# Performance work log

Measured on AMD Instinct MI355X. Metric: run time of the kernel, lower is better.

## Reference

```python
import jax, jax.numpy as jnp
import numpy as np

EPS = 1e-5

def _layer_norm(x, w, b):
    mu = jnp.mean(x, axis=-1, keepdims=True)
    var = jnp.mean(jnp.square(x - mu), axis=-1, keepdims=True)
    return (x - mu) * jax.lax.rsqrt(var + EPS) * w + b

def setup_inputs() -> dict:
    key = jax.random.key(0)
    ks = jax.random.split(key, 5)
    B, S, C = 1, 512, 128
    scale = 1.0 / np.sqrt(C)
    return {
        "z_ij": jax.random.normal(ks[0], (B, S, S, C), dtype=jnp.float32),
        "ln_w": jnp.ones((C,), jnp.float32),
        "ln_b": jnp.zeros((C,), jnp.float32),
        "wa": jax.random.normal(ks[1], (C, C), dtype=jnp.float32) * scale,
        "wb": jax.random.normal(ks[2], (C, C), dtype=jnp.float32) * scale,
        "wg": jax.random.normal(ks[3], (C, C), dtype=jnp.float32) * scale,
        "fln_w": jnp.ones((C,), jnp.float32),
        "fln_b": jnp.zeros((C,), jnp.float32),
        "wf": jax.random.normal(ks[4], (C, C), dtype=jnp.float32) * scale,
    }

def reference(z_ij, ln_w, ln_b, wa, wb, wg, fln_w, fln_b, wf):
    # z_ij: (B, S, S, C). torch Linear(x) == x @ W.T
    z = _layer_norm(z_ij, ln_w, ln_b)
    a = jax.nn.sigmoid(z @ wa.T)  # (B, S, S, C)
    b = jax.nn.sigmoid(z @ wb.T)
    g = jax.nn.sigmoid(z @ wg.T)
    # torch: einsum('...kic,...kjc->...ijc', a.transpose(-3,-2), b)
    # == out[i,j,c] = sum_k a[i,k,c] * b[k,j,c]
    p = jnp.einsum('bikc,bkjc->bijc', a, b)
    return g * (_layer_norm(p, fln_w, fln_b) @ wf.T)
```

## Files before the change

kernel.cpp:

```cpp
#include <hip/hip_runtime.h>

#define SS 512
#define CC 128
#define RR (SS*SS)

typedef unsigned short u16;
typedef unsigned int   u32;
typedef __attribute__((ext_vector_type(4))) float f32x4;
typedef __attribute__((ext_vector_type(8))) short s16x8;
typedef __attribute__((ext_vector_type(4))) u32   u32x4;

__device__ __forceinline__ float bf2f(u16 u){ u32 x = ((u32)u)<<16; float f; __builtin_memcpy(&f,&x,4); return f; }
__device__ __forceinline__ float sigf(float x){ return 1.f/(1.f + __expf(-x)); }

__device__ __forceinline__ u32 cvtpk(float lo, float hi){
  u32 r; asm("v_cvt_pk_bf16_f32 %0, %1, %2" : "=v"(r) : "v"(lo), "v"(hi)); return r;
}

typedef __attribute__((address_space(1))) void* gptr_t;
typedef __attribute__((address_space(3))) void* lptr_t;
__device__ __forceinline__ void load_lds16(const void* g, void* l){
  __builtin_amdgcn_global_load_lds((gptr_t)(g), (lptr_t)(l), 16, 0, 0);
}

__global__ void k0(const float* __restrict__ wa, const float* __restrict__ wb,
                   const float* __restrict__ wg, const float* __restrict__ wf,
                   u16* __restrict__ wabg, u16* __restrict__ wfbg)
{
  int t = blockIdx.x*256 + threadIdx.x;
  const float* srcs[4] = {wa, wb, wg, wf};
  int m = t >> 11;
  int e = (t & 2047) * 8;
  const float* s = srcs[m] + e;
  u32 pk[4];
  #pragma unroll
  for (int v=0; v<2; v++){
    f32x4 x = *reinterpret_cast<const f32x4*>(s + v*4);
    pk[v*2]   = cvtpk(x[0], x[1]);
    pk[v*2+1] = cvtpk(x[2], x[3]);
  }
  u16* dst = (m==3) ? (wfbg + e) : (wabg + m*16384 + e);
  *reinterpret_cast<u32x4*>(dst) = *reinterpret_cast<u32x4*>(pk);
}

__global__ __launch_bounds__(256,4) void k1(
    const float* __restrict__ z, const float* __restrict__ lnw, const float* __restrict__ lnb,
    const u16* __restrict__ wabg,
    u16* __restrict__ a_t, u16* __restrict__ b_t, u16* __restrict__ g_out,
    float* __restrict__ SaPart)
{
  __shared__ __align__(16) u16 un[9216];
  __shared__ __align__(16) u16 wk[64*128];
  u16 (*zn)[136] = reinterpret_cast<u16(*)[136]>(un);
  u16* tr = un;
  const int tid = threadIdx.x;
  const int r0  = blockIdx.x * 64;
  const int lane = tid & 63, w = tid >> 6;
  const int iI   = r0 >> 9;
  const int kblk = (r0 >> 6) & 7;

  auto stageW = [&](int m, int h){
    const u16* Wb = wabg + m*16384 + h*8192;
    #pragma unroll
    for (int s=0;s<4;s++){
      int lr = s*16 + (tid>>4);
      const u16* gsrc = Wb + lr*128 + (((tid&15) ^ (lr&7))<<3);
      load_lds16((const void*)gsrc, (void*)&wk[s*2048 + w*512]);
    }
  };

  stageW(0,0);

  {
    int row = tid >> 2, q = tid & 3;
    const float* src = z + (size_t)(r0+row)*CC + q*32;
    float v[32]; float s = 0.f, s2 = 0.f;
    #pragma unroll
    for (int i=0;i<8;i++){
      f32x4 t = *reinterpret_cast<const f32x4*>(src + i*4);
      #pragma unroll
      for (int e=0;e<4;e++){ float x = t[e]; v[i*4+e]=x; s += x; s2 += x*x; }
    }
    s  += __shfl_xor(s,1);  s2 += __shfl_xor(s2,1);
    s  += __shfl_xor(s,2);  s2 += __shfl_xor(s2,2);
    float mu  = s * (1.f/128.f);
    float var = s2*(1.f/128.f) - mu*mu;
    float rs  = rsqrtf(var + 1e-5f);
    #pragma unroll
    for (int i=0;i<4;i++){
      u32 pk[4];
      #pragma unroll
      for (int e=0;e<8;e+=2){
        int ci = i*8+e; int c = q*32 + ci;
        float y0 = (v[ci]  -mu)*rs*lnw[c]   + lnb[c];
        float y1 = (v[ci+1]-mu)*rs*lnw[c+1] + lnb[c+1];
        pk[e>>1] = cvtpk(y0, y1);
      }
      *reinterpret_cast<u32x4*>(&zn[row][q*32 + i*8]) = *reinterpret_cast<u32x4*>(pk);
    }
  }
  __syncthreads();

  s16x8 af[4];
  #pragma unroll
  for (int ks=0;ks<4;ks++)
    af[ks] = *reinterpret_cast<const s16x8*>(&zn[w*16 + (lane&15)][ks*32 + (lane>>4)*8]);

  for (int m=0;m<3;m++){
    f32x4 acc[8];
    #pragma unroll
    for (int cb=0;cb<8;cb++) acc[cb] = (f32x4){0.f,0.f,0.f,0.f};

    #pragma unroll
    for (int cb=0;cb<4;cb++){
      int lr = cb*16 + (lane&15);
      const int rx = (lr&7)<<3;
      const u16* base = &wk[lr*128];
      s16x8 b0 = *reinterpret_cast<const s16x8*>(&base[(  0 + (lane>>4)*8) ^ rx]);
      s16x8 b1 = *reinterpret_cast<const s16x8*>(&base[( 32 + (lane>>4)*8) ^ rx]);
      s16x8 b2 = *reinterpret_cast<const s16x8*>(&base[( 64 + (lane>>4)*8) ^ rx]);
      s16x8 b3 = *reinterpret_cast<const s16x8*>(&base[( 96 + (lane>>4)*8) ^ rx]);
      acc[cb] = __builtin_amdgcn_mfma_f32_16x16x32_bf16(af[0], b0, acc[cb], 0,0,0);
      acc[cb] = __builtin_amdgcn_mfma_f32_16x16x32_bf16(af[1], b1, acc[cb], 0,0,0);
      acc[cb] = __builtin_amdgcn_mfma_f32_16x16x32_bf16(af[2], b2, acc[cb], 0,0,0);
      acc[cb] = __builtin_amdgcn_mfma_f32_16x16x32_bf16(af[3], b3, acc[cb], 0,0,0);
    }
    __syncthreads();
    stageW(m,1);
    __syncthreads();

    #pragma unroll
    for (int cb=4;cb<8;cb++){
      int lr = (cb-4)*16 + (lane&15);
      const int rx = (lr&7)<<3;
      const u16* base = &wk[lr*128];
      s16x8 b0 = *reinterpret_cast<const s16x8*>(&base[(  0 + (lane>>4)*8) ^ rx]);
      s16x8 b1 = *reinterpret_cast<const s16x8*>(&base[( 32 + (lane>>4)*8) ^ rx]);
      s16x8 b2 = *reinterpret_cast<const s16x8*>(&base[( 64 + (lane>>4)*8) ^ rx]);
      s16x8 b3 = *reinterpret_cast<const s16x8*>(&base[( 96 + (lane>>4)*8) ^ rx]);
      acc[cb] = __builtin_amdgcn_mfma_f32_16x16x32_bf16(af[0], b0, acc[cb], 0,0,0);
      acc[cb] = __builtin_amdgcn_mfma_f32_16x16x32_bf16(af[1], b1, acc[cb], 0,0,0);
      acc[cb] = __builtin_amdgcn_mfma_f32_16x16x32_bf16(af[2], b2, acc[cb], 0,0,0);
      acc[cb] = __builtin_amdgcn_mfma_f32_16x16x32_bf16(af[3], b3, acc[cb], 0,0,0);
    }
    __syncthreads();

    if (m<2) stageW(m+1,0);

    if (m < 2){
      #pragma unroll
      for (int cb=0;cb<8;cb++){
        int col = cb*16 + (lane&15);
        int rbase = w*16 + (lane>>4)*4;
        u32 p0 = cvtpk(sigf(acc[cb][0])-0.5f, sigf(acc[cb][1])-0.5f);
        u32 p1 = cvtpk(sigf(acc[cb][2])-0.5f, sigf(acc[cb][3])-0.5f);
        u32* d = reinterpret_cast<u32*>(&tr[col*72 + rbase]);
        d[0] = p0; d[1] = p1;
      }
      asm volatile("s_waitcnt lgkmcnt(0)" ::: "memory");
      __builtin_amdgcn_s_barrier();
      {
        int c = tid>>1, half = tid&1;
        u16* dst = (m==0 ? a_t : b_t) + ((size_t)c<<18) + r0 + half*32;
        const u16* srcl = &tr[c*72 + half*32];
        float s = 0.f;
        #pragma unroll
        for (int e=0;e<4;e++){
          u32x4 t = *reinterpret_cast<const u32x4*>(srcl + e*8);
          *reinterpret_cast<u32x4*>(dst + e*8) = t;
          #pragma unroll
          for (int q=0;q<4;q++){ u32 v = t[q]; s += bf2f((u16)v) + bf2f((u16)(v>>16)); }
        }
        if (m==0){
          s += __shfl_xor(s, 1);
          if ((tid&1)==0) SaPart[(kblk<<16) + (iI<<7) + c] = s;
        }
      }
      __syncthreads();
    } else {
      u16* gb = &tr[0];
      #pragma unroll
      for (int cb=0;cb<8;cb++){
        int col = cb*16 + (lane&15);
        int rbase = w*16 + (lane>>4)*4;
        #pragma unroll
        for (int q=0;q<4;q++){
          float sg = sigf(acc[cb][q]);
          gb[(rbase+q)*136 + col] = (u16)cvtpk(sg, sg);
        }
      }
      asm volatile("s_waitcnt lgkmcnt(0)" ::: "memory");
      __builtin_amdgcn_s_barrier();
      {
        int row = tid>>2, qo = tid&3;
        u16* dst = g_out + (size_t)(r0+row)*CC + qo*32;
        const u16* srcl = &gb[row*136 + qo*32];
        #pragma unroll
        for (int e=0;e<4;e++)
          *reinterpret_cast<u32x4*>(dst + e*8) = *reinterpret_cast<const u32x4*>(srcl + e*8);
      }
    }
  }
}

__global__ __launch_bounds__(256,4) void k1b(const u16* __restrict__ b_t, u16* __restrict__ bT,
                                             float* __restrict__ SbPart)
{
  __shared__ __align__(16) u16 tile[64][72];
  const int tid = threadIdx.x;
  const int c  = blockIdx.x >> 6;
  const int t  = blockIdx.x & 63;
  const int k0 = (t>>3)*64, j0 = (t&7)*64;
  const u16* src = b_t + ((size_t)c<<18);
  {
    int row = tid>>3, chunk = tid&7;
    #pragma unroll
    for (int pass=0; pass<2; pass++){
      int k = row + pass*32;
      const u16* s = src + (size_t)(k0+k)*SS + j0 + chunk*8;
      u32x4 v = *reinterpret_cast<const u32x4*>(s);
      int cs = chunk ^ ((k>>3)&7);
      *reinterpret_cast<u32x4*>(&tile[k][cs*8]) = v;
    }
  }
  __syncthreads();
  {
    int j = tid>>2, part = tid&3;
    u32 pk[8];
    float sb = 0.f;
    #pragma unroll
    for (int i=0;i<16;i+=2){
      int ka = part*16 + i;
      int key = (ka>>3)&7;
      u16 va = tile[ka  ][(((j>>3)^key)*8) + (j&7)];
      u16 vb = tile[ka+1][(((j>>3)^key)*8) + (j&7)];
      pk[i>>1] = (u32)va | ((u32)vb<<16);
      sb += bf2f(va) + bf2f(vb);
    }
    u16* dst = bT + ((size_t)c<<18) + (size_t)(j0+j)*SS + k0 + part*16;
    *reinterpret_cast<u32x4*>(dst)   = *reinterpret_cast<u32x4*>(pk);
    *reinterpret_cast<u32x4*>(dst+8) = *reinterpret_cast<u32x4*>(pk+4);
    sb += __shfl_xor(sb, 1);
    sb += __shfl_xor(sb, 2);
    if (part==0) SbPart[(((c<<9) + j0 + j)<<3) + (k0>>6)] = sb;
  }
}

__global__ void k1c(const float* __restrict__ SaPart, const float* __restrict__ SbPart,
                    float* __restrict__ Sa, float* __restrict__ Sb)
{
  int idx = blockIdx.x*256 + threadIdx.x;
  if (idx < 65536){
    int i = idx >> 7, c = idx & 127;
    float s = 0.f;
    #pragma unroll
    for (int b=0;b<8;b++) s += SaPart[(b<<16) + (i<<7) + c];
    Sa[(c<<9) + i] = s;
  } else {
    int cj = idx & 65535;
    const float* src = SbPart + ((size_t)cj << 3);
    float s = 0.f;
    #pragma unroll
    for (int b=0;b<8;b++) s += src[b];
    Sb[cj] = s;
  }
}

__global__ __launch_bounds__(256,2) void k2(const u16* __restrict__ a_t, const u16* __restrict__ bT,
                                            const float* __restrict__ Sa, const float* __restrict__ Sb,
                                            _Float16* __restrict__ ph)
{
  __shared__ __align__(16) u16 As[2][128*64];
  __shared__ __align__(16) u16 Bs[128*64];
  const int tid = threadIdx.x;
  const int lane = tid & 63, w = tid >> 6;
  const int bid = blockIdx.x;
  const int swz = (bid & 7) * 256 + (bid >> 3);
  const int c   = swz >> 4;
  const int t16 = swz & 15;
  const int i0 = (t16 >> 2) * 128, j0 = (t16 & 3) * 128;
  const u16* Ag = a_t + ((size_t)c<<18);
  const u16* Bg = bT  + ((size_t)c<<18);
  const int pr = lane>>3, slot = lane&7;

  auto stageA = [&](int kt, int buf){
    #pragma unroll
    for (int s=0;s<4;s++){
      int rbase = w*32 + s*8;
      int rl = rbase + pr;
      const u16* g = Ag + (size_t)(i0+rl)*SS + kt*64 + ((slot^pr)*8);
      load_lds16((const void*)g, (void*)&As[buf][rbase*64]);
    }
  };
  auto stageB = [&](int kt){
    #pragma unroll
    for (int s=0;s<4;s++){
      int rbase = w*32 + s*8;
      int rl = rbase + pr;
      const u16* g = Bg + (size_t)(j0+rl)*SS + kt*64 + ((slot^pr)*8);
      load_lds16((const void*)g, (void*)&Bs[rbase*64]);
    }
  };

  f32x4 acc[4][4];
  #pragma unroll
  for (int a=0;a<4;a++)
    #pragma unroll
    for (int b=0;b<4;b++) acc[a][b] = (f32x4){0.f,0.f,0.f,0.f};
  const int wr = w>>1, wc = w&1;

  stageA(0, 0);
  for (int kt=0; kt<8; ++kt){
    stageB(kt);
    if (kt < 7){
      stageA(kt+1, (kt+1)&1);
      asm volatile("s_waitcnt vmcnt(4)" ::: "memory");
    } else {
      asm volatile("s_waitcnt vmcnt(0)" ::: "memory");
    }
    __builtin_amdgcn_s_barrier();
    const u16* Ab = &As[kt&1][0];
    #pragma unroll
    for (int ks=0;ks<2;ks++){
      s16x8 af[4], bfv[4];
      #pragma unroll
      for (int f=0; f<4; f++){
        int i = wr*64 + f*16 + (lane&15);
        int ch = (ks*4 + (lane>>4)) ^ (i&7);
        af[f] = *reinterpret_cast<const s16x8*>(&Ab[i*64 + ch*8]);
        int j = wc*64 + f*16 + (lane&15);
        int chb = (ks*4 + (lane>>4)) ^ (j&7);
        bfv[f] = *reinterpret_cast<const s16x8*>(&Bs[j*64 + chb*8]);
      }
      #pragma unroll
      for (int fi=0;fi<4;fi++)
        #pragma unroll
        for (int fj=0;fj<4;fj++)
          acc[fi][fj] = __builtin_amdgcn_mfma_f32_16x16x32_bf16(af[fi], bfv[fj], acc[fi][fj], 0,0,0);
    }
    asm volatile("s_waitcnt lgkmcnt(0)" ::: "memory");
    __builtin_amdgcn_s_barrier();
  }

  _Float16* P = ph + ((size_t)c<<18);
  const float* SaC = Sa + (c<<9);
  const float* SbC = Sb + (c<<9);
  float sbv[4];
  #pragma unroll
  for (int fj=0;fj<4;fj++) sbv[fj] = SbC[j0 + wc*64 + fj*16 + (lane&15)];
  #pragma unroll
  for (int fi=0;fi<4;fi++){
    int rbase = i0 + wr*64 + fi*16 + (lane>>4)*4;
    #pragma unroll
    for (int q=0;q<4;q++){
      float sav = SaC[rbase+q];
      #pragma unroll
      for (int fj=0;fj<4;fj++){
        int col = j0 + wc*64 + fj*16 + (lane&15);
        P[(size_t)(rbase+q)*SS + col] = (_Float16)(0.5f*(sav + sbv[fj]) + acc[fi][fj][q]);
      }
    }
  }
}

__global__ __launch_bounds__(256,3) void k3(const _Float16* __restrict__ ph, const u16* __restrict__ g,
    const float* __restrict__ flnw, const float* __restrict__ flnb,
    const u16* __restrict__ wfbg, float* __restrict__ out)
{
  __shared__ __align__(16) u16 znp[64][136];
  __shared__ __align__(16) u16 wk[128*128];
  __shared__ __align__(16) float red[4][64];
  __shared__ __align__(16) float muv[64], rsv[64];
  const int tid = threadIdx.x;
  const int rr0 = blockIdx.x * 64;
  const int lane = tid&63, w = tid>>6;
  const int pos = tid & 63, cq = tid >> 6;

  {
    #pragma unroll
    for (int s=0;s<8;s++){
      int row = s*16 + (tid>>4);
      const u16* gsrc = wfbg + row*128 + (((tid&15) ^ (row&7))<<3);
      load_lds16((const void*)gsrc, (void*)&wk[s*2048 + w*512]);
    }
  }

  float pv[32];
  {
    const _Float16* src = ph + rr0 + pos;
    float s = 0.f;
    #pragma unroll
    for (int ci=0;ci<32;ci++){
      int c = cq*32 + ci;
      float x = (float)src[((size_t)c)<<18];
      pv[ci] = x; s += x;
    }
    red[cq][pos] = s;
  }
  __syncthreads();
  if (tid < 64) muv[tid] = (red[0][tid]+red[1][tid]+red[2][tid]+red[3][tid]) * (1.f/128.f);
  __syncthreads();
  float mu = muv[pos];
  {
    float s2 = 0.f;
    #pragma unroll
    for (int ci=0;ci<32;ci++){ float d = pv[ci]-mu; s2 += d*d; }
    red[cq][pos] = s2;
  }
  __syncthreads();
  if (tid < 64) rsv[tid] = rsqrtf((red[0][tid]+red[1][tid]+red[2][tid]+red[3][tid])*(1.f/128.f) + 1e-5f);
  __syncthreads();
  float rs = rsv[pos];
  {
    u32 pk[4];
    #pragma unroll
    for (int ii=0;ii<4;ii++){
      #pragma unroll
      for (int e=0;e<8;e+=2){
        int ci = ii*8+e; int c = cq*32+ci;
        float y0 = (pv[ci]  -mu)*rs*flnw[c]   + flnb[c];
        float y1 = (pv[ci+1]-mu)*rs*flnw[c+1] + flnb[c+1];
        pk[e>>1] = cvtpk(y0, y1);
      }
      *reinterpret_cast<u32x4*>(&znp[pos][cq*32 + ii*8]) = *reinterpret_cast<u32x4*>(pk);
    }
  }
  __syncthreads();

  f32x4 acc[8];
  #pragma unroll
  for (int cb=0;cb<8;cb++) acc[cb] = (f32x4){0.f,0.f,0.f,0.f};
  #pragma unroll
  for (int ks=0;ks<4;ks++){
    s16x8 af = *reinterpret_cast<const s16x8*>(&znp[w*16 + (lane&15)][ks*32 + (lane>>4)*8]);
    #pragma unroll
    for (int cb=0;cb<8;cb++){
      int row = cb*16 + (lane&15);
      const int rx = (row&7)<<3;
      s16x8 bf = *reinterpret_cast<const s16x8*>(&wk[row*128 + ((ks*32 + (lane>>4)*8) ^ rx)]);
      acc[cb] = __builtin_amdgcn_mfma_f32_16x16x32_bf16(af, bf, acc[cb], 0,0,0);
    }
  }
  __syncthreads();

  u16* gb = &znp[0][0];
  {
    int row = tid>>2, qo = tid&3;
    const u16* src = g + (size_t)(rr0+row)*CC + qo*32;
    #pragma unroll
    for (int e=0;e<4;e++)
      *reinterpret_cast<u32x4*>(&gb[row*136 + qo*32 + e*8]) = *reinterpret_cast<const u32x4*>(src + e*8);
  }
  __syncthreads();
  #pragma unroll
  for (int cb=0;cb<8;cb++){
    int col = cb*16 + (lane&15);
    int rbase = w*16 + (lane>>4)*4;
    #pragma unroll
    for (int q=0;q<4;q++){
      float gv = bf2f(gb[(rbase+q)*136 + col]);
      out[(size_t)(rr0+rbase+q)*CC + col] = gv * acc[cb][q];
    }
  }
}

extern "C" void kernel_launch(void* const* d_in, const int* in_sizes, int n_in,
                              void* d_out, int out_size, void* d_ws, size_t ws_size,
                              hipStream_t stream)
{
  const float* z    = (const float*)d_in[0];
  const float* lnw  = (const float*)d_in[1];
  const float* lnb  = (const float*)d_in[2];
  const float* wa   = (const float*)d_in[3];
  const float* wb   = (const float*)d_in[4];
  const float* wg   = (const float*)d_in[5];
  const float* flnw = (const float*)d_in[6];
  const float* flnb = (const float*)d_in[7];
  const float* wf   = (const float*)d_in[8];
  float* out = (float*)d_out;

  char* ws = (char*)d_ws;
  u16* a_t = (u16*)(ws);
  u16* bT  = (u16*)(ws + ((size_t)64<<20));
  u16* g   = (u16*)(ws + ((size_t)128<<20));
  _Float16* ph = (_Float16*)(ws + ((size_t)192<<20));
  u16* b_t = (u16*)(ws + ((size_t)192<<20));
  u16* wfbg = (u16*)(ws + ((size_t)256<<20));

  char* ob = (char*)d_out;
  u16*   wabg   = (u16*)ob;
  float* SaPart = (float*)(ob + ((size_t)1<<20));
  float* SbPart = (float*)(ob + ((size_t)3<<20));
  float* Sa     = (float*)(ob + ((size_t)5<<20));
  float* Sb     = (float*)(ob + ((size_t)5<<20) + ((size_t)256<<10));

  k0 <<<32,   256, 0, stream>>>(wa, wb, wg, wf, wabg, wfbg);
  k1 <<<4096, 256, 0, stream>>>(z, lnw, lnb, wabg, a_t, b_t, g, SaPart);
  k1b<<<8192, 256, 0, stream>>>(b_t, bT, SbPart);
  k1c<<<512,  256, 0, stream>>>(SaPart, SbPart, Sa, Sb);
  k2 <<<2048, 256, 0, stream>>>(a_t, bT, Sa, Sb, ph);
  k3 <<<4096, 256, 0, stream>>>(ph, g, flnw, flnb, wfbg, out);
}
```

Measured before the change: 276.6 us.

## Shrink weight LDS staging in k1/k3 and raise occupancy launch bounds

k1 now streams each 128x128 gate weight into LDS in four 32-row quarters instead of two 64-row halves, and k3 streams Wf in two halves instead of all at once. Both changes shrink the shared-memory footprint so more blocks can be resident per CU. Launch-bound minimum-occupancy hints are raised on k1, k1b, k2 and k3. The cost is more barriers and weight reloads that are exposed without overlap, plus a risk of register spills under the tighter register limits.

Result: slower. 296.4 us (+7.1%).

```diff
diff --git a/kernel.cpp b/kernel.cpp
--- a/kernel.cpp
+++ b/kernel.cpp
@@ -43,14 +43,14 @@
   *reinterpret_cast<u32x4*>(dst) = *reinterpret_cast<u32x4*>(pk);
 }
 
-__global__ __launch_bounds__(256,4) void k1(
+__global__ __launch_bounds__(256,6) void k1(
     const float* __restrict__ z, const float* __restrict__ lnw, const float* __restrict__ lnb,
     const u16* __restrict__ wabg,
     u16* __restrict__ a_t, u16* __restrict__ b_t, u16* __restrict__ g_out,
     float* __restrict__ SaPart)
 {
   __shared__ __align__(16) u16 un[9216];
-  __shared__ __align__(16) u16 wk[64*128];
+  __shared__ __align__(16) u16 wk[32*128];
   u16 (*zn)[136] = reinterpret_cast<u16(*)[136]>(un);
   u16* tr = un;
   const int tid = threadIdx.x;
@@ -59,10 +59,10 @@
   const int iI   = r0 >> 9;
   const int kblk = (r0 >> 6) & 7;
 
-  auto stageW = [&](int m, int h){
-    const u16* Wb = wabg + m*16384 + h*8192;
-    #pragma unroll
-    for (int s=0;s<4;s++){
+  auto stageW = [&](int m, int qt){
+    const u16* Wb = wabg + m*16384 + qt*4096;
+    #pragma unroll
+    for (int s=0;s<2;s++){
       int lr = s*16 + (tid>>4);
       const u16* gsrc = Wb + lr*128 + (((tid&15) ^ (lr&7))<<3);
       load_lds16((const void*)gsrc, (void*)&wk[s*2048 + w*512]);
@@ -111,41 +111,26 @@
     #pragma unroll
     for (int cb=0;cb<8;cb++) acc[cb] = (f32x4){0.f,0.f,0.f,0.f};
 
-    #pragma unroll
-    for (int cb=0;cb<4;cb++){
-      int lr = cb*16 + (lane&15);
-      const int rx = (lr&7)<<3;
-      const u16* base = &wk[lr*128];
-      s16x8 b0 = *reinterpret_cast<const s16x8*>(&base[(  0 + (lane>>4)*8) ^ rx]);
-      s16x8 b1 = *reinterpret_cast<const s16x8*>(&base[( 32 + (lane>>4)*8) ^ rx]);
-      s16x8 b2 = *reinterpret_cast<const s16x8*>(&base[( 64 + (lane>>4)*8) ^ rx]);
-      s16x8 b3 = *reinterpret_cast<const s16x8*>(&base[( 96 + (lane>>4)*8) ^ rx]);
-      acc[cb] = __builtin_amdgcn_mfma_f32_16x16x32_bf16(af[0], b0, acc[cb], 0,0,0);
-      acc[cb] = __builtin_amdgcn_mfma_f32_16x16x32_bf16(af[1], b1, acc[cb], 0,0,0);
-      acc[cb] = __builtin_amdgcn_mfma_f32_16x16x32_bf16(af[2], b2, acc[cb], 0,0,0);
-      acc[cb] = __builtin_amdgcn_mfma_f32_16x16x32_bf16(af[3], b3, acc[cb], 0,0,0);
-    }
-    __syncthreads();
-    stageW(m,1);
-    __syncthreads();
-
-    #pragma unroll
-    for (int cb=4;cb<8;cb++){
-      int lr = (cb-4)*16 + (lane&15);
-      const int rx = (lr&7)<<3;
-      const u16* base = &wk[lr*128];
-      s16x8 b0 = *reinterpret_cast<const s16x8*>(&base[(  0 + (lane>>4)*8) ^ rx]);
-      s16x8 b1 = *reinterpret_cast<const s16x8*>(&base[( 32 + (lane>>4)*8) ^ rx]);
-      s16x8 b2 = *reinterpret_cast<const s16x8*>(&base[( 64 + (lane>>4)*8) ^ rx]);
-      s16x8 b3 = *reinterpret_cast<const s16x8*>(&base[( 96 + (lane>>4)*8) ^ rx]);
-      acc[cb] = __builtin_amdgcn_mfma_f32_16x16x32_bf16(af[0], b0, acc[cb], 0,0,0);
-      acc[cb] = __builtin_amdgcn_mfma_f32_16x16x32_bf16(af[1], b1, acc[cb], 0,0,0);
-      acc[cb] = __builtin_amdgcn_mfma_f32_16x16x32_bf16(af[2], b2, acc[cb], 0,0,0);
-      acc[cb] = __builtin_amdgcn_mfma_f32_16x16x32_bf16(af[3], b3, acc[cb], 0,0,0);
-    }
-    __syncthreads();
-
-    if (m<2) stageW(m+1,0);
+    for (int qt=0; qt<4; ++qt){
+      __syncthreads();
+      #pragma unroll
+      for (int cc=0; cc<2; ++cc){
+        int cb = qt*2 + cc;
+        int lr = cc*16 + (lane&15);
+        const int rx = (lr&7)<<3;
+        const u16* base = &wk[lr*128];
+        s16x8 b0 = *reinterpret_cast<const s16x8*>(&base[(  0 + (lane>>4)*8) ^ rx]);
+        s16x8 b1 = *reinterpret_cast<const s16x8*>(&base[( 32 + (lane>>4)*8) ^ rx]);
+        s16x8 b2 = *reinterpret_cast<const s16x8*>(&base[( 64 + (lane>>4)*8) ^ rx]);
+        s16x8 b3 = *reinterpret_cast<const s16x8*>(&base[( 96 + (lane>>4)*8) ^ rx]);
+        acc[cb] = __builtin_amdgcn_mfma_f32_16x16x32_bf16(af[0], b0, acc[cb], 0,0,0);
+        acc[cb] = __builtin_amdgcn_mfma_f32_16x16x32_bf16(af[1], b1, acc[cb], 0,0,0);
+        acc[cb] = __builtin_amdgcn_mfma_f32_16x16x32_bf16(af[2], b2, acc[cb], 0,0,0);
+        acc[cb] = __builtin_amdgcn_mfma_f32_16x16x32_bf16(af[3], b3, acc[cb], 0,0,0);
+      }
+      __syncthreads();
+      if (qt<3) stageW(m, qt+1);
+    }
 
     if (m < 2){
       #pragma unroll
@@ -157,8 +142,8 @@
         u32* d = reinterpret_cast<u32*>(&tr[col*72 + rbase]);
         d[0] = p0; d[1] = p1;
       }
-      asm volatile("s_waitcnt lgkmcnt(0)" ::: "memory");
-      __builtin_amdgcn_s_barrier();
+      __syncthreads();
+      stageW(m+1, 0);
       {
         int c = tid>>1, half = tid&1;
         u16* dst = (m==0 ? a_t : b_t) + ((size_t)c<<18) + r0 + half*32;
@@ -189,8 +174,7 @@
           gb[(rbase+q)*136 + col] = (u16)cvtpk(sg, sg);
         }
       }
-      asm volatile("s_waitcnt lgkmcnt(0)" ::: "memory");
-      __builtin_amdgcn_s_barrier();
+      __syncthreads();
       {
         int row = tid>>2, qo = tid&3;
         u16* dst = g_out + (size_t)(r0+row)*CC + qo*32;
@@ -203,7 +187,7 @@
   }
 }
 
-__global__ __launch_bounds__(256,4) void k1b(const u16* __restrict__ b_t, u16* __restrict__ bT,
+__global__ __launch_bounds__(256,8) void k1b(const u16* __restrict__ b_t, u16* __restrict__ bT,
                                              float* __restrict__ SbPart)
 {
   __shared__ __align__(16) u16 tile[64][72];
@@ -266,7 +250,7 @@
   }
 }
 
-__global__ __launch_bounds__(256,2) void k2(const u16* __restrict__ a_t, const u16* __restrict__ bT,
+__global__ __launch_bounds__(256,3) void k2(const u16* __restrict__ a_t, const u16* __restrict__ bT,
                                             const float* __restrict__ Sa, const float* __restrict__ Sb,
                                             _Float16* __restrict__ ph)
 {
@@ -363,12 +347,12 @@
   }
 }
 
-__global__ __launch_bounds__(256,3) void k3(const _Float16* __restrict__ ph, const u16* __restrict__ g,
+__global__ __launch_bounds__(256,4) void k3(const _Float16* __restrict__ ph, const u16* __restrict__ g,
     const float* __restrict__ flnw, const float* __restrict__ flnb,
     const u16* __restrict__ wfbg, float* __restrict__ out)
 {
   __shared__ __align__(16) u16 znp[64][136];
-  __shared__ __align__(16) u16 wk[128*128];
+  __shared__ __align__(16) u16 wk[64*128];
   __shared__ __align__(16) float red[4][64];
   __shared__ __align__(16) float muv[64], rsv[64];
   const int tid = threadIdx.x;
@@ -376,14 +360,17 @@
   const int lane = tid&63, w = tid>>6;
   const int pos = tid & 63, cq = tid >> 6;
 
-  {
-    #pragma unroll
-    for (int s=0;s<8;s++){
-      int row = s*16 + (tid>>4);
-      const u16* gsrc = wfbg + row*128 + (((tid&15) ^ (row&7))<<3);
+  auto stageWF = [&](int h){
+    const u16* Wb = wfbg + h*8192;
+    #pragma unroll
+    for (int s=0;s<4;s++){
+      int lr = s*16 + (tid>>4);
+      const u16* gsrc = Wb + lr*128 + (((tid&15) ^ (lr&7))<<3);
       load_lds16((const void*)gsrc, (void*)&wk[s*2048 + w*512]);
     }
-  }
+  };
+
+  stageWF(0);
 
   float pv[32];
   {
@@ -430,14 +417,30 @@
   f32x4 acc[8];
   #pragma unroll
   for (int cb=0;cb<8;cb++) acc[cb] = (f32x4){0.f,0.f,0.f,0.f};
+
   #pragma unroll
   for (int ks=0;ks<4;ks++){
     s16x8 af = *reinterpret_cast<const s16x8*>(&znp[w*16 + (lane&15)][ks*32 + (lane>>4)*8]);
     #pragma unroll
-    for (int cb=0;cb<8;cb++){
-      int row = cb*16 + (lane&15);
-      const int rx = (row&7)<<3;
-      s16x8 bf = *reinterpret_cast<const s16x8*>(&wk[row*128 + ((ks*32 + (lane>>4)*8) ^ rx)]);
+    for (int cb=0;cb<4;cb++){
+      int lr = cb*16 + (lane&15);
+      const int rx = (lr&7)<<3;
+      s16x8 bf = *reinterpret_cast<const s16x8*>(&wk[lr*128 + ((ks*32 + (lane>>4)*8) ^ rx)]);
+      acc[cb] = __builtin_amdgcn_mfma_f32_16x16x32_bf16(af, bf, acc[cb], 0,0,0);
+    }
+  }
+  __syncthreads();
+  stageWF(1);
+  __syncthreads();
+
+  #pragma unroll
+  for (int ks=0;ks<4;ks++){
+    s16x8 af = *reinterpret_cast<const s16x8*>(&znp[w*16 + (lane&15)][ks*32 + (lane>>4)*8]);
+    #pragma unroll
+    for (int cb=4;cb<8;cb++){
+      int lr = (cb-4)*16 + (lane&15);
+      const int rx = (lr&7)<<3;
+      s16x8 bf = *reinterpret_cast<const s16x8*>(&wk[lr*128 + ((ks*32 + (lane>>4)*8) ^ rx)]);
       acc[cb] = __builtin_amdgcn_mfma_f32_16x16x32_bf16(af, bf, acc[cb], 0,0,0);
     }
   }
```

## Store gate in channel-major layout and raise occupancy bounds on k1b and k2

Applied to the files above, without the earlier changes.

The gate tensor g is now written in the same channel-major transposed layout as a and b, reusing the shared transpose path in k1 instead of a separate row-major branch. k3 reads it back channel-major into a 72-stride LDS tile and indexes it transposed. The row-sum accumulation is now limited to m==0, so it no longer runs for the b pass. Launch bounds rise to 8 waves for k1b and 3 for k2, which can add register pressure or spills.

Measured after the change: 278.4 us. About the same (+0.6%).

```diff
diff --git a/kernel.cpp b/kernel.cpp
--- a/kernel.cpp
+++ b/kernel.cpp
@@ -147,63 +147,48 @@
 
     if (m<2) stageW(m+1,0);
 
-    if (m < 2){
+    {
       #pragma unroll
       for (int cb=0;cb<8;cb++){
         int col = cb*16 + (lane&15);
         int rbase = w*16 + (lane>>4)*4;
-        u32 p0 = cvtpk(sigf(acc[cb][0])-0.5f, sigf(acc[cb][1])-0.5f);
-        u32 p1 = cvtpk(sigf(acc[cb][2])-0.5f, sigf(acc[cb][3])-0.5f);
+        u32 p0, p1;
+        if (m < 2){
+          p0 = cvtpk(sigf(acc[cb][0])-0.5f, sigf(acc[cb][1])-0.5f);
+          p1 = cvtpk(sigf(acc[cb][2])-0.5f, sigf(acc[cb][3])-0.5f);
+        } else {
+          p0 = cvtpk(sigf(acc[cb][0]), sigf(acc[cb][1]));
+          p1 = cvtpk(sigf(acc[cb][2]), sigf(acc[cb][3]));
+        }
         u32* d = reinterpret_cast<u32*>(&tr[col*72 + rbase]);
         d[0] = p0; d[1] = p1;
       }
-      asm volatile("s_waitcnt lgkmcnt(0)" ::: "memory");
-      __builtin_amdgcn_s_barrier();
+      __syncthreads();
       {
         int c = tid>>1, half = tid&1;
-        u16* dst = (m==0 ? a_t : b_t) + ((size_t)c<<18) + r0 + half*32;
+        u16* dst = (m==0 ? a_t : (m==1 ? b_t : g_out)) + ((size_t)c<<18) + r0 + half*32;
         const u16* srcl = &tr[c*72 + half*32];
         float s = 0.f;
         #pragma unroll
         for (int e=0;e<4;e++){
           u32x4 t = *reinterpret_cast<const u32x4*>(srcl + e*8);
           *reinterpret_cast<u32x4*>(dst + e*8) = t;
-          #pragma unroll
-          for (int q=0;q<4;q++){ u32 v = t[q]; s += bf2f((u16)v) + bf2f((u16)(v>>16)); }
+          if (m==0){
+            #pragma unroll
+            for (int q=0;q<4;q++){ u32 v = t[q]; s += bf2f((u16)v) + bf2f((u16)(v>>16)); }
+          }
         }
         if (m==0){
           s += __shfl_xor(s, 1);
           if ((tid&1)==0) SaPart[(kblk<<16) + (iI<<7) + c] = s;
         }
       }
-      __syncthreads();
-    } else {
-      u16* gb = &tr[0];
-      #pragma unroll
-      for (int cb=0;cb<8;cb++){
-        int col = cb*16 + (lane&15);
-        int rbase = w*16 + (lane>>4)*4;
-        #pragma unroll
-        for (int q=0;q<4;q++){
-          float sg = sigf(acc[cb][q]);
-          gb[(rbase+q)*136 + col] = (u16)cvtpk(sg, sg);
-        }
-      }
-      asm volatile("s_waitcnt lgkmcnt(0)" ::: "memory");
-      __builtin_amdgcn_s_barrier();
-      {
-        int row = tid>>2, qo = tid&3;
-        u16* dst = g_out + (size_t)(r0+row)*CC + qo*32;
-        const u16* srcl = &gb[row*136 + qo*32];
-        #pragma unroll
-        for (int e=0;e<4;e++)
-          *reinterpret_cast<u32x4*>(dst + e*8) = *reinterpret_cast<const u32x4*>(srcl + e*8);
-      }
-    }
-  }
-}
-
-__global__ __launch_bounds__(256,4) void k1b(const u16* __restrict__ b_t, u16* __restrict__ bT,
+      if (m<2) __syncthreads();
+    }
+  }
+}
+
+__global__ __launch_bounds__(256,8) void k1b(const u16* __restrict__ b_t, u16* __restrict__ bT,
                                              float* __restrict__ SbPart)
 {
   __shared__ __align__(16) u16 tile[64][72];
@@ -266,7 +251,7 @@
   }
 }
 
-__global__ __launch_bounds__(256,2) void k2(const u16* __restrict__ a_t, const u16* __restrict__ bT,
+__global__ __launch_bounds__(256,3) void k2(const u16* __restrict__ a_t, const u16* __restrict__ bT,
                                             const float* __restrict__ Sa, const float* __restrict__ Sb,
                                             _Float16* __restrict__ ph)
 {
@@ -367,10 +352,11 @@
     const float* __restrict__ flnw, const float* __restrict__ flnb,
     const u16* __restrict__ wfbg, float* __restrict__ out)
 {
-  __shared__ __align__(16) u16 znp[64][136];
+  __shared__ __align__(16) u16 un[9216];
   __shared__ __align__(16) u16 wk[128*128];
   __shared__ __align__(16) float red[4][64];
   __shared__ __align__(16) float muv[64], rsv[64];
+  u16 (*znp)[136] = reinterpret_cast<u16(*)[136]>(un);
   const int tid = threadIdx.x;
   const int rr0 = blockIdx.x * 64;
   const int lane = tid&63, w = tid>>6;
@@ -443,13 +429,14 @@
   }
   __syncthreads();
 
-  u16* gb = &znp[0][0];
-  {
-    int row = tid>>2, qo = tid&3;
-    const u16* src = g + (size_t)(rr0+row)*CC + qo*32;
+  u16* gb = un;
+  {
+    int c = tid>>1, half = tid&1;
+    const u16* src = g + ((size_t)c<<18) + rr0 + half*32;
+    u16* dstl = &gb[c*72 + half*32];
     #pragma unroll
     for (int e=0;e<4;e++)
-      *reinterpret_cast<u32x4*>(&gb[row*136 + qo*32 + e*8]) = *reinterpret_cast<const u32x4*>(src + e*8);
+      *reinterpret_cast<u32x4*>(dstl + e*8) = *reinterpret_cast<const u32x4*>(src + e*8);
   }
   __syncthreads();
   #pragma unroll
@@ -458,7 +445,7 @@
     int rbase = w*16 + (lane>>4)*4;
     #pragma unroll
     for (int q=0;q<4;q++){
-      float gv = bf2f(gb[(rbase+q)*136 + col]);
+      float gv = bf2f(gb[col*72 + rbase + q]);
       out[(size_t)(rr0+rbase+q)*CC + col] = gv * acc[cb][q];
     }
   }
```
